# Kernel tuning notes

Measured on AMD Instinct MI355X. Metric: run time of the kernel, lower is better.

## Reference

```python
import jax, jax.numpy as jnp
import numpy as np

B, S, DM, H, FF = 2, 2048, 1024, 16, 4096
DH = DM // H
EPS = 1e-5


def setup_inputs() -> dict:
    key = jax.random.key(0)
    ks = jax.random.split(key, 16)
    s = 0.02
    return {
        "x": jax.random.normal(ks[0], (B, S, DM), jnp.float32),
        "mask": jnp.ones((B, S), jnp.int32),
        "Wq": jax.random.normal(ks[1], (DM, DM), jnp.float32) * s,
        "bq": jnp.zeros((DM,), jnp.float32),
        "Wk": jax.random.normal(ks[2], (DM, DM), jnp.float32) * s,
        "bk": jnp.zeros((DM,), jnp.float32),
        "Wv": jax.random.normal(ks[3], (DM, DM), jnp.float32) * s,
        "bv": jnp.zeros((DM,), jnp.float32),
        "Wo": jax.random.normal(ks[4], (DM, DM), jnp.float32) * s,
        "bo": jnp.zeros((DM,), jnp.float32),
        "W1": jax.random.normal(ks[5], (DM, FF), jnp.float32) * s,
        "b1": jnp.zeros((FF,), jnp.float32),
        "W2": jax.random.normal(ks[6], (FF, DM), jnp.float32) * s,
        "b2": jnp.zeros((DM,), jnp.float32),
        "g1": jnp.ones((DM,), jnp.float32),
        "beta1": jnp.zeros((DM,), jnp.float32),
        "g2": jnp.ones((DM,), jnp.float32),
        "beta2": jnp.zeros((DM,), jnp.float32),
    }


def _layer_norm(x, g, b):
    mu = jnp.mean(x, axis=-1, keepdims=True)
    var = jnp.var(x, axis=-1, keepdims=True)
    return (x - mu) * jax.lax.rsqrt(var + EPS) * g + b


def reference(x, mask, Wq, bq, Wk, bk, Wv, bv, Wo, bo, W1, b1, W2, b2, g1, beta1, g2, beta2):
    # --- hollow multi-head attention ---
    q = (x @ Wq + bq).reshape(B, S, H, DH)
    k = (x @ Wk + bk).reshape(B, S, H, DH)
    v = (x @ Wv + bv).reshape(B, S, H, DH)
    scores = jnp.einsum("bqhd,bkhd->bhqk", q, k) / jnp.sqrt(jnp.float32(DH))
    # triu(diag=1) and tril(diag=-1) masks kill everything off-diagonal
    diag = jnp.eye(S, dtype=bool)  # [S, S]
    scores = jnp.where(diag[None, None], scores, -jnp.inf)
    attn = jax.nn.softmax(scores, axis=-1)
    out = jnp.einsum("bhqk,bkhd->bqhd", attn, v).reshape(B, S, DM)
    attn_out = out @ Wo + bo
    # --- residual + LN1 ---
    h = _layer_norm(x + attn_out, g1, beta1)
    # --- FFN ---
    ff = jax.nn.relu(h @ W1 + b1) @ W2 + b2
    # --- residual + LN2 ---
    return _layer_norm(h + ff, g2, beta2)
```

## Files before the change

kernel.cpp:

```cpp
#include <hip/hip_runtime.h>
#include <stdint.h>

typedef __bf16 bf16x8 __attribute__((ext_vector_type(8)));
typedef float f32x4 __attribute__((ext_vector_type(4)));

__device__ __forceinline__ uint16_t f2bf(float f) {
  union { float f; uint32_t u; } c; c.f = f;
  uint32_t u = c.u;
  u += 0x7fffu + ((u >> 16) & 1u);
  return (uint16_t)(u >> 16);
}
__device__ __forceinline__ float bf2f(uint16_t u) {
  union { uint32_t u; float f; } c; c.u = (uint32_t)u << 16; return c.f;
}

__device__ __forceinline__ void cvt_body(const float* __restrict__ in,
                                         uint16_t* __restrict__ out, int i) {
  float4 v = reinterpret_cast<const float4*>(in)[i];
  ushort4 o;
  o.x = f2bf(v.x); o.y = f2bf(v.y); o.z = f2bf(v.z); o.w = f2bf(v.w);
  reinterpret_cast<ushort4*>(out)[i] = o;
}

__global__ void prep_kernel(const float* __restrict__ x, const float* __restrict__ Wv,
                            const float* __restrict__ Wo, const float* __restrict__ W1,
                            const float* __restrict__ W2, const float* __restrict__ bv,
                            const float* __restrict__ bo,
                            uint16_t* __restrict__ xb, uint16_t* __restrict__ wvb,
                            uint16_t* __restrict__ woT, uint16_t* __restrict__ w1t,
                            uint16_t* __restrict__ w2t, float* __restrict__ bc) {
  __shared__ float tsh[32][33];
  __shared__ float red[8][32];
  int b = blockIdx.x;
  const int t = threadIdx.x;
  if (b < 4096) { cvt_body(x, xb, b * 256 + t); return; }
  b -= 4096;
  if (b < 1024) { cvt_body(Wv, wvb, b * 256 + t); return; }
  b -= 1024;

  const float* tin = nullptr; uint16_t* tout = nullptr;
  int R = 0, C = 0, bx = 0, by = 0;
  if (b < 1024) {
    tin = Wo; tout = woT; R = 1024; C = 1024; bx = b & 31; by = b >> 5;
  } else if (b < 1024 + 4096) {
    const int bb = b - 1024;
    tin = W1; tout = w1t; R = 1024; C = 4096; bx = bb & 127; by = bb >> 7;
  } else if (b < 1024 + 8192) {
    const int bb = b - (1024 + 4096);
    tin = W2; tout = w2t; R = 4096; C = 1024; bx = bb & 31; by = bb >> 5;
  } else {
    const int jb = b - (1024 + 8192);
    const int jl = t & 31, kg = t >> 5;
    const int j = jb * 32 + jl;
    float s = 0.f;
    const int k0 = kg * 128;
    for (int k = k0; k < k0 + 128; ++k) s += bv[k] * Wo[(size_t)k * 1024 + j];
    red[kg][jl] = s;
    __syncthreads();
    if (kg == 0) {
      float acc = bo[j];
#pragma unroll
      for (int q = 0; q < 8; ++q) acc += red[q][jl];
      bc[j] = acc;
    }
    return;
  }
  const int tx = t & 31, ty = t >> 5;
  const int c0 = bx * 32, r0 = by * 32;
#pragma unroll
  for (int i = 0; i < 4; ++i)
    tsh[ty + i * 8][tx] = tin[(size_t)(r0 + ty + i * 8) * C + (c0 + tx)];
  __syncthreads();
#pragma unroll
  for (int i = 0; i < 4; ++i)
    tout[(size_t)(c0 + ty + i * 8) * R + (r0 + tx)] = f2bf(tsh[tx][ty + i * 8]);
}

constexpr int BM = 128, BN = 128, BK = 64;

template <int MODE>
__launch_bounds__(256, 2)
__global__ void gemm2ph_kernel(const uint16_t* __restrict__ A, const uint16_t* __restrict__ Bt,
                               const float* __restrict__ bias, const float* __restrict__ res,
                               void* __restrict__ out, int M, int N, int Klen, int lda, int ldb) {
  __shared__ uint16_t sAB[2][2][BM * BK];
  const int tid  = threadIdx.x;
  const int lane = tid & 63;
  const int wave = tid >> 6;

  const int nwg = gridDim.x * gridDim.y;
  int wg = blockIdx.y * gridDim.x + blockIdx.x;
  wg = (wg & 7) * (nwg >> 3) + (wg >> 3);
  const int bx = wg % gridDim.x, by = wg / gridDim.x;
  const int m0 = by * BM, n0 = bx * BN;

  const int wm = (wave >> 1) * 64;
  const int wn = (wave & 1) * 64;

  f32x4 acc[4][4] = {};

  const int srow = tid >> 3;
  const int scol = ((tid & 7) ^ (srow & 7)) * 8;
  const uint16_t* ga[4];
  const uint16_t* gb[4];
  uint32_t loff[4];
#pragma unroll
  for (int g = 0; g < 4; ++g) {
    const int row = srow + 32 * g;
    ga[g] = A + (size_t)(m0 + row) * lda + scol;
    gb[g] = Bt + (size_t)(n0 + row) * ldb + scol;
    loff[g] = (uint32_t)(tid + g * 256) * 8;
  }

  const int fr = lane & 15;
  const int hi = lane >> 4;
  const int rx = fr & 7;

  const int nk = Klen / BK;

#define STAGE2(buf, kt)                                                                   \
  {                                                                                       \
    _Pragma("unroll")                                                                     \
    for (int g = 0; g < 4; ++g) {                                                         \
      __builtin_amdgcn_global_load_lds(                                                   \
          (const __attribute__((address_space(1))) uint32_t*)(ga[g] + (size_t)(kt) * BK), \
          (__attribute__((address_space(3))) uint32_t*)(&sAB[buf][0][loff[g]]), 16, 0, 0);\
      __builtin_amdgcn_global_load_lds(                                                   \
          (const __attribute__((address_space(1))) uint32_t*)(gb[g] + (size_t)(kt) * BK), \
          (__attribute__((address_space(3))) uint32_t*)(&sAB[buf][1][loff[g]]), 16, 0, 0);\
    }                                                                                     \
  }

  STAGE2(0, 0);
  __syncthreads();

  int cur = 0;
  for (int kt = 0; kt < nk; ++kt) {
    if (kt + 1 < nk) STAGE2(cur ^ 1, kt + 1);
    const uint16_t* pA = &sAB[cur][0][0];
    const uint16_t* pB = &sAB[cur][1][0];
    bf16x8 af[4][2], bb[4][2];
#pragma unroll
    for (int m = 0; m < 4; ++m)
#pragma unroll
      for (int ks = 0; ks < 2; ++ks) {
        const int slot = (ks * 4 + hi) ^ rx;
        af[m][ks] = *reinterpret_cast<const bf16x8*>(pA + (wm + m * 16 + fr) * BK + slot * 8);
        bb[m][ks] = *reinterpret_cast<const bf16x8*>(pB + (wn + m * 16 + fr) * BK + slot * 8);
      }
#pragma unroll
    for (int ks = 0; ks < 2; ++ks)
#pragma unroll
      for (int m = 0; m < 4; ++m)
#pragma unroll
        for (int n = 0; n < 4; ++n)
          acc[m][n] = __builtin_amdgcn_mfma_f32_16x16x32_bf16(af[m][ks], bb[n][ks], acc[m][n], 0, 0, 0);
    __syncthreads();
    cur ^= 1;
  }
#undef STAGE2

  const int cn  = lane & 15;
  const int cm4 = (lane >> 4) * 4;
#pragma unroll
  for (int m = 0; m < 4; ++m) {
#pragma unroll
    for (int n = 0; n < 4; ++n) {
      const int gm = m0 + wm + m * 16 + cm4;
      const int gn = n0 + wn + n * 16 + cn;
      const float bbv = bias ? bias[gn] : 0.f;
#pragma unroll
      for (int r = 0; r < 4; ++r) {
        const size_t idx = (size_t)(gm + r) * N + gn;
        const float vv = acc[m][n][r] + bbv;
        if constexpr (MODE == 0) {
          ((uint16_t*)out)[idx] = f2bf(vv);
        } else {
          ((uint16_t*)out)[idx] = f2bf(vv + res[idx]);
        }
      }
    }
  }
}

template <int MODE>
__launch_bounds__(512, 2)
__global__ void gemm8ph_kernel(const uint16_t* __restrict__ A, const uint16_t* __restrict__ Bt,
                               const float* __restrict__ bias, void* __restrict__ out,
                               int M, int N, int Klen, int lda, int ldb) {
  extern __shared__ uint16_t lds[];
  const int tid  = threadIdx.x;
  const int lane = tid & 63;
  const int wave = tid >> 6;

  const int nwg = gridDim.x * gridDim.y;
  int wg = blockIdx.y * gridDim.x + blockIdx.x;
  wg = (wg & 7) * (nwg >> 3) + (wg >> 3);
  const int bx = wg % gridDim.x, by = wg / gridDim.x;
  const int m0 = by * 256, n0 = bx * 256;

  const int z = blockIdx.z;
  A  += (size_t)z * Klen;
  Bt += (size_t)z * Klen;

  const int wm = (wave >> 2) * 128;
  const int wn = (wave & 3) * 64;

  f32x4 acc[8][4] = {};

  const int srw = tid >> 3;
  const int sp  = tid & 7;
  const uint16_t* gu[8];
#pragma unroll
  for (int u = 0; u < 8; ++u) {
    const uint16_t* base = (u < 4) ? A + (size_t)(m0 + u * 64) * lda
                                   : Bt + (size_t)(n0 + (u - 4) * 64) * ldb;
    const int ld = (u < 4) ? lda : ldb;
    gu[u] = base + (size_t)srw * ld + ((sp ^ (srw & 7)) * 8);
  }

  const int nk = Klen / 64;

#define STAGE8(T, U)                                                                          \
  if ((T) < nk) {                                                                             \
    __builtin_amdgcn_global_load_lds(                                                         \
        (const __attribute__((address_space(1))) uint32_t*)(gu[U] + (size_t)(T) * 64),        \
        (__attribute__((address_space(3))) uint32_t*)(lds + ((T) & 1) * 32768 + (U) * 4096 +  \
                                                      tid * 8),                               \
        16, 0, 0);                                                                            \
  }

  const int fr = lane & 15;
  const int hi = lane >> 4;
  int aoff[8];
#pragma unroll
  for (int m = 0; m < 8; ++m) {
    const int u = (wm >> 6) + (m >> 2);
    const int R = (m & 3) * 16 + fr;
    aoff[m] = u * 4096 + R * 64 + ((hi ^ (R & 7)) * 8);
  }
  int boff[4];
#pragma unroll
  for (int n = 0; n < 4; ++n) {
    const int u = 4 + (wn >> 6);
    const int R = n * 16 + fr;
    boff[n] = u * 4096 + R * 64 + ((hi ^ (R & 7)) * 8);
  }

  STAGE8(0, 0); STAGE8(0, 1); STAGE8(0, 2); STAGE8(0, 3);
  STAGE8(0, 4); STAGE8(0, 5); STAGE8(0, 6); STAGE8(0, 7);
  STAGE8(1, 4); STAGE8(1, 5); STAGE8(1, 6); STAGE8(1, 7);
  asm volatile("s_waitcnt vmcnt(4)" ::: "memory");
  __builtin_amdgcn_s_barrier();

#define LD8(off) (*reinterpret_cast<const bf16x8*>(bufp + (off)))
#define PHASE_MFMA32(KS)                                                      \
  __builtin_amdgcn_s_setprio(1);                                              \
  _Pragma("unroll") for (int mm = 0; mm < 8; ++mm)                            \
    _Pragma("unroll") for (int n = 0; n < 4; ++n)                             \
      acc[mm][n] = __builtin_amdgcn_mfma_f32_16x16x32_bf16(                   \
          aq[mm], bq[n][KS], acc[mm][n], 0, 0, 0);                            \
  __builtin_amdgcn_s_setprio(0);

  for (int k = 0; k < nk; ++k) {
    const uint16_t* bufp = lds + (k & 1) * 32768;
    bf16x8 bq[4][2], aq[8];
#pragma unroll
    for (int n = 0; n < 4; ++n) { bq[n][0] = LD8(boff[n]); bq[n][1] = LD8(boff[n] ^ 32); }
#pragma unroll
    for (int mm = 0; mm < 8; ++mm) aq[mm] = LD8(aoff[mm]);
    STAGE8(k + 1, 0); STAGE8(k + 1, 1); STAGE8(k + 1, 2); STAGE8(k + 1, 3);
    PHASE_MFMA32(0);
    asm volatile("s_waitcnt lgkmcnt(0)" ::: "memory");
    __builtin_amdgcn_s_barrier();
#pragma unroll
    for (int mm = 0; mm < 8; ++mm) aq[mm] = LD8(aoff[mm] ^ 32);
    STAGE8(k + 2, 4); STAGE8(k + 2, 5); STAGE8(k + 2, 6); STAGE8(k + 2, 7);
    PHASE_MFMA32(1);
    if (k < nk - 2) { asm volatile("s_waitcnt vmcnt(4)" ::: "memory"); }
    else            { asm volatile("s_waitcnt vmcnt(0)" ::: "memory"); }
    asm volatile("s_waitcnt lgkmcnt(0)" ::: "memory");
    __builtin_amdgcn_s_barrier();
  }
#undef PHASE_MFMA32
#undef LD8
#undef STAGE8

  const int cn  = lane & 15;
  const int cm4 = (lane >> 4) * 4;
  uint16_t* outp = (uint16_t*)out;
  if constexpr (MODE == 1) outp += (size_t)z * M * N;
  float bias_n[4];
  if constexpr (MODE == 0) {
#pragma unroll
    for (int n = 0; n < 4; ++n) bias_n[n] = bias[n0 + wn + n * 16 + cn];
  }
#pragma unroll
  for (int m = 0; m < 8; ++m) {
#pragma unroll
    for (int n = 0; n < 4; ++n) {
      const int gm = m0 + wm + m * 16 + cm4;
      const int gn = n0 + wn + n * 16 + cn;
#pragma unroll
      for (int r = 0; r < 4; ++r) {
        const size_t idx = (size_t)(gm + r) * N + gn;
        if constexpr (MODE == 0) {
          outp[idx] = f2bf(fmaxf(acc[m][n][r] + bias_n[n], 0.f));
        } else {
          outp[idx] = f2bf(acc[m][n][r]);
        }
      }
    }
  }
}

__global__ void ln1_kernel(const uint16_t* __restrict__ in,
                           const float* __restrict__ g,
                           const float* __restrict__ b,
                           uint16_t* __restrict__ outb) {
  const int row = blockIdx.x;
  const int t = threadIdx.x;
  const ushort4 r4 = reinterpret_cast<const ushort4*>(in + (size_t)row * 1024)[t];
  float4 v;
  v.x = bf2f(r4.x); v.y = bf2f(r4.y); v.z = bf2f(r4.z); v.w = bf2f(r4.w);
  float s  = v.x + v.y + v.z + v.w;
  float s2 = v.x * v.x + v.y * v.y + v.z * v.z + v.w * v.w;
#pragma unroll
  for (int o = 32; o > 0; o >>= 1) { s += __shfl_down(s, o); s2 += __shfl_down(s2, o); }
  __shared__ float red[8];
  const int lane = t & 63, wave = t >> 6;
  if (lane == 0) { red[wave] = s; red[4 + wave] = s2; }
  __syncthreads();
  const float S  = red[0] + red[1] + red[2] + red[3];
  const float S2 = red[4] + red[5] + red[6] + red[7];
  const float mu  = S * (1.f / 1024.f);
  const float var = S2 * (1.f / 1024.f) - mu * mu;
  const float rs  = rsqrtf(var + 1e-5f);
  const float4 gg = reinterpret_cast<const float4*>(g)[t];
  const float4 bb = reinterpret_cast<const float4*>(b)[t];
  ushort4 ob;
  ob.x = f2bf((v.x - mu) * rs * gg.x + bb.x);
  ob.y = f2bf((v.y - mu) * rs * gg.y + bb.y);
  ob.z = f2bf((v.z - mu) * rs * gg.z + bb.z);
  ob.w = f2bf((v.w - mu) * rs * gg.w + bb.w);
  reinterpret_cast<ushort4*>(outb + (size_t)row * 1024)[t] = ob;
}

__global__ void ln2_kernel(const uint16_t* __restrict__ pp, size_t pstride,
                           const uint16_t* __restrict__ hb, const float* __restrict__ b2,
                           const float* __restrict__ g, const float* __restrict__ be,
                           float* __restrict__ out) {
  const int row = blockIdx.x;
  const int t = threadIdx.x;
  const size_t base = (size_t)row * 1024;
  const ushort4 h4 = reinterpret_cast<const ushort4*>(hb + base)[t];
  const float4 c2 = reinterpret_cast<const float4*>(b2)[t];
  float4 v;
  v.x = c2.x + bf2f(h4.x); v.y = c2.y + bf2f(h4.y);
  v.z = c2.z + bf2f(h4.z); v.w = c2.w + bf2f(h4.w);
#pragma unroll
  for (int zz = 0; zz < 4; ++zz) {
    const ushort4 p4 = reinterpret_cast<const ushort4*>(pp + zz * pstride + base)[t];
    v.x += bf2f(p4.x); v.y += bf2f(p4.y); v.z += bf2f(p4.z); v.w += bf2f(p4.w);
  }
  float s  = v.x + v.y + v.z + v.w;
  float s2 = v.x * v.x + v.y * v.y + v.z * v.z + v.w * v.w;
#pragma unroll
  for (int o = 32; o > 0; o >>= 1) { s += __shfl_down(s, o); s2 += __shfl_down(s2, o); }
  __shared__ float red[8];
  const int lane = t & 63, wave = t >> 6;
  if (lane == 0) { red[wave] = s; red[4 + wave] = s2; }
  __syncthreads();
  const float S  = red[0] + red[1] + red[2] + red[3];
  const float S2 = red[4] + red[5] + red[6] + red[7];
  const float mu  = S * (1.f / 1024.f);
  const float var = S2 * (1.f / 1024.f) - mu * mu;
  const float rs  = rsqrtf(var + 1e-5f);
  const float4 gg = reinterpret_cast<const float4*>(g)[t];
  const float4 bb = reinterpret_cast<const float4*>(be)[t];
  float4 o;
  o.x = (v.x - mu) * rs * gg.x + bb.x;
  o.y = (v.y - mu) * rs * gg.y + bb.y;
  o.z = (v.z - mu) * rs * gg.z + bb.z;
  o.w = (v.w - mu) * rs * gg.w + bb.w;
  reinterpret_cast<float4*>(out + base)[t] = o;
}

extern "C" void kernel_launch(void* const* d_in, const int* in_sizes, int n_in,
                              void* d_out, int out_size, void* d_ws, size_t ws_size,
                              hipStream_t stream) {
  const float* x   = (const float*)d_in[0];
  const float* Wv  = (const float*)d_in[6];
  const float* bv  = (const float*)d_in[7];
  const float* Wo  = (const float*)d_in[8];
  const float* bo  = (const float*)d_in[9];
  const float* W1  = (const float*)d_in[10];
  const float* b1  = (const float*)d_in[11];
  const float* W2  = (const float*)d_in[12];
  const float* b2  = (const float*)d_in[13];
  const float* g1  = (const float*)d_in[14];
  const float* be1 = (const float*)d_in[15];
  const float* g2  = (const float*)d_in[16];
  const float* be2 = (const float*)d_in[17];
  float* out = (float*)d_out;

  constexpr int M = 4096, DM = 1024, FF = 4096;

  char* p = (char*)d_ws;
  auto alloc = [&](size_t bytes) {
    char* r = p;
    p += (bytes + 255) & ~(size_t)255;
    return r;
  };
  uint16_t* xb  = (uint16_t*)alloc((size_t)M * DM * 2);
  uint16_t* wvb = (uint16_t*)alloc((size_t)DM * DM * 2);
  uint16_t* woT = (uint16_t*)alloc((size_t)DM * DM * 2);
  uint16_t* w1t = (uint16_t*)alloc((size_t)FF * DM * 2);
  uint16_t* w2t = (uint16_t*)alloc((size_t)DM * FF * 2);
  uint16_t* wcT = (uint16_t*)alloc((size_t)DM * DM * 2);
  float*    bc  = (float*)   alloc((size_t)DM * 4);
  uint16_t* r1b = (uint16_t*)alloc((size_t)M * DM * 2);
  uint16_t* hb  = (uint16_t*)alloc((size_t)M * DM * 2);
  uint16_t* tb  = (uint16_t*)alloc((size_t)M * FF * 2);
  uint16_t* pp  = (uint16_t*)alloc((size_t)4 * M * DM * 2);

  (void)hipFuncSetAttribute(reinterpret_cast<const void*>(gemm8ph_kernel<0>),
                            hipFuncAttributeMaxDynamicSharedMemorySize, 131072);
  (void)hipFuncSetAttribute(reinterpret_cast<const void*>(gemm8ph_kernel<1>),
                            hipFuncAttributeMaxDynamicSharedMemorySize, 131072);

  prep_kernel<<<4096 + 1024 + 1024 + 4096 + 4096 + 32, 256, 0, stream>>>(
      x, Wv, Wo, W1, W2, bv, bo, xb, wvb, woT, w1t, w2t, bc);

  gemm2ph_kernel<0><<<dim3(DM / BN, DM / BM), 256, 0, stream>>>(
      woT, wvb, nullptr, nullptr, wcT, DM, DM, DM, DM, DM);
  gemm2ph_kernel<1><<<dim3(DM / BN, M / BM), 256, 0, stream>>>(
      xb, wcT, bc, x, r1b, M, DM, DM, DM, DM);
  ln1_kernel<<<M, 256, 0, stream>>>(r1b, g1, be1, hb);
  gemm8ph_kernel<0><<<dim3(FF / 256, M / 256), 512, 131072, stream>>>(
      hb, w1t, b1, tb, M, FF, DM, DM, DM);
  gemm8ph_kernel<1><<<dim3(DM / 256, M / 256, 4), 512, 131072, stream>>>(
      tb, w2t, nullptr, pp, M, DM, FF / 4, FF, FF);
  ln2_kernel<<<M, 256, 0, stream>>>(pp, (size_t)M * DM, hb, b2, g2, be2, out);
}
```

Measured before the change: 143.2 us.

## Replace 256x256 FFN GEMM with smaller-tile, higher-occupancy 128x256 kernel

The FFN GEMMs move from a 256x256 tile with 128KB of dynamic LDS and a two-phase K=64 pipeline to a 128x256 tile with K=32 steps and static double-buffered LDS of 48KB. Launch bounds rise to 4 blocks per CU and the grid doubles in the M dimension. The aim is more resident waves to hide latency and better CU fill for these fairly small GEMMs. In exchange, per-tile reuse drops and the loop waits for all loads with vmcnt(0) on every iteration, so there is more global traffic and less overlap inside each block.

New measurement: 150.8 us. 5.4% more time.

```diff
diff --git a/kernel.cpp b/kernel.cpp
--- a/kernel.cpp
+++ b/kernel.cpp
@@ -184,11 +184,12 @@
 }
 
 template <int MODE>
-__launch_bounds__(512, 2)
-__global__ void gemm8ph_kernel(const uint16_t* __restrict__ A, const uint16_t* __restrict__ Bt,
+__launch_bounds__(512, 4)
+__global__ void gemm_hi_kernel(const uint16_t* __restrict__ A, const uint16_t* __restrict__ Bt,
                                const float* __restrict__ bias, void* __restrict__ out,
                                int M, int N, int Klen, int lda, int ldb) {
-  extern __shared__ uint16_t lds[];
+  __shared__ uint16_t sA[2][128 * 32];
+  __shared__ uint16_t sB[2][256 * 32];
   const int tid  = threadIdx.x;
   const int lane = tid & 63;
   const int wave = tid >> 6;
@@ -197,94 +198,77 @@
   int wg = blockIdx.y * gridDim.x + blockIdx.x;
   wg = (wg & 7) * (nwg >> 3) + (wg >> 3);
   const int bx = wg % gridDim.x, by = wg / gridDim.x;
-  const int m0 = by * 256, n0 = bx * 256;
+  const int m0 = by * 128, n0 = bx * 256;
 
   const int z = blockIdx.z;
   A  += (size_t)z * Klen;
   Bt += (size_t)z * Klen;
 
-  const int wm = (wave >> 2) * 128;
+  const int wm = (wave >> 2) * 64;
   const int wn = (wave & 3) * 64;
 
-  f32x4 acc[8][4] = {};
-
-  const int srw = tid >> 3;
-  const int sp  = tid & 7;
-  const uint16_t* gu[8];
-#pragma unroll
-  for (int u = 0; u < 8; ++u) {
-    const uint16_t* base = (u < 4) ? A + (size_t)(m0 + u * 64) * lda
-                                   : Bt + (size_t)(n0 + (u - 4) * 64) * ldb;
-    const int ld = (u < 4) ? lda : ldb;
-    gu[u] = base + (size_t)srw * ld + ((sp ^ (srw & 7)) * 8);
-  }
-
-  const int nk = Klen / 64;
-
-#define STAGE8(T, U)                                                                          \
-  if ((T) < nk) {                                                                             \
-    __builtin_amdgcn_global_load_lds(                                                         \
-        (const __attribute__((address_space(1))) uint32_t*)(gu[U] + (size_t)(T) * 64),        \
-        (__attribute__((address_space(3))) uint32_t*)(lds + ((T) & 1) * 32768 + (U) * 4096 +  \
-                                                      tid * 8),                               \
-        16, 0, 0);                                                                            \
+  f32x4 acc[4][4] = {};
+
+  const int srw = tid >> 2;
+  const int sp  = tid & 3;
+  const int skey = (srw >> 1) & 3;
+  const uint16_t* gA  = A  + (size_t)(m0 + srw) * lda + ((sp ^ skey) * 8);
+  const uint16_t* gB0 = Bt + (size_t)(n0 + srw) * ldb + ((sp ^ skey) * 8);
+  const uint16_t* gB1 = gB0 + (size_t)128 * ldb;
+
+  const int nk = Klen / 32;
+
+#define STG(T, buf)                                                                         \
+  {                                                                                         \
+    __builtin_amdgcn_global_load_lds(                                                       \
+        (const __attribute__((address_space(1))) uint32_t*)(gA + (size_t)(T) * 32),         \
+        (__attribute__((address_space(3))) uint32_t*)(&sA[buf][tid * 8]), 16, 0, 0);        \
+    __builtin_amdgcn_global_load_lds(                                                       \
+        (const __attribute__((address_space(1))) uint32_t*)(gB0 + (size_t)(T) * 32),        \
+        (__attribute__((address_space(3))) uint32_t*)(&sB[buf][tid * 8]), 16, 0, 0);        \
+    __builtin_amdgcn_global_load_lds(                                                       \
+        (const __attribute__((address_space(1))) uint32_t*)(gB1 + (size_t)(T) * 32),        \
+        (__attribute__((address_space(3))) uint32_t*)(&sB[buf][(tid + 512) * 8]), 16, 0, 0);\
   }
 
   const int fr = lane & 15;
   const int hi = lane >> 4;
-  int aoff[8];
-#pragma unroll
-  for (int m = 0; m < 8; ++m) {
-    const int u = (wm >> 6) + (m >> 2);
-    const int R = (m & 3) * 16 + fr;
-    aoff[m] = u * 4096 + R * 64 + ((hi ^ (R & 7)) * 8);
-  }
-  int boff[4];
+  int aoff[4], boff[4];
+#pragma unroll
+  for (int m = 0; m < 4; ++m) {
+    const int R = wm + m * 16 + fr;
+    aoff[m] = R * 32 + ((hi ^ ((R >> 1) & 3)) * 8);
+  }
 #pragma unroll
   for (int n = 0; n < 4; ++n) {
-    const int u = 4 + (wn >> 6);
-    const int R = n * 16 + fr;
-    boff[n] = u * 4096 + R * 64 + ((hi ^ (R & 7)) * 8);
-  }
-
-  STAGE8(0, 0); STAGE8(0, 1); STAGE8(0, 2); STAGE8(0, 3);
-  STAGE8(0, 4); STAGE8(0, 5); STAGE8(0, 6); STAGE8(0, 7);
-  STAGE8(1, 4); STAGE8(1, 5); STAGE8(1, 6); STAGE8(1, 7);
-  asm volatile("s_waitcnt vmcnt(4)" ::: "memory");
+    const int R = wn + n * 16 + fr;
+    boff[n] = R * 32 + ((hi ^ ((R >> 1) & 3)) * 8);
+  }
+
+  STG(0, 0);
+  asm volatile("s_waitcnt vmcnt(0)" ::: "memory");
   __builtin_amdgcn_s_barrier();
 
-#define LD8(off) (*reinterpret_cast<const bf16x8*>(bufp + (off)))
-#define PHASE_MFMA32(KS)                                                      \
-  __builtin_amdgcn_s_setprio(1);                                              \
-  _Pragma("unroll") for (int mm = 0; mm < 8; ++mm)                            \
-    _Pragma("unroll") for (int n = 0; n < 4; ++n)                             \
-      acc[mm][n] = __builtin_amdgcn_mfma_f32_16x16x32_bf16(                   \
-          aq[mm], bq[n][KS], acc[mm][n], 0, 0, 0);                            \
-  __builtin_amdgcn_s_setprio(0);
-
   for (int k = 0; k < nk; ++k) {
-    const uint16_t* bufp = lds + (k & 1) * 32768;
-    bf16x8 bq[4][2], aq[8];
-#pragma unroll
-    for (int n = 0; n < 4; ++n) { bq[n][0] = LD8(boff[n]); bq[n][1] = LD8(boff[n] ^ 32); }
-#pragma unroll
-    for (int mm = 0; mm < 8; ++mm) aq[mm] = LD8(aoff[mm]);
-    STAGE8(k + 1, 0); STAGE8(k + 1, 1); STAGE8(k + 1, 2); STAGE8(k + 1, 3);
-    PHASE_MFMA32(0);
+    const int cur = k & 1;
+    if (k + 1 < nk) STG(k + 1, cur ^ 1);
+    bf16x8 aq[4], bq[4];
+#pragma unroll
+    for (int m = 0; m < 4; ++m) aq[m] = *reinterpret_cast<const bf16x8*>(&sA[cur][aoff[m]]);
+#pragma unroll
+    for (int n = 0; n < 4; ++n) bq[n] = *reinterpret_cast<const bf16x8*>(&sB[cur][boff[n]]);
+    __builtin_amdgcn_s_setprio(1);
+#pragma unroll
+    for (int m = 0; m < 4; ++m)
+#pragma unroll
+      for (int n = 0; n < 4; ++n)
+        acc[m][n] = __builtin_amdgcn_mfma_f32_16x16x32_bf16(aq[m], bq[n], acc[m][n], 0, 0, 0);
+    __builtin_amdgcn_s_setprio(0);
+    asm volatile("s_waitcnt vmcnt(0)" ::: "memory");
     asm volatile("s_waitcnt lgkmcnt(0)" ::: "memory");
     __builtin_amdgcn_s_barrier();
-#pragma unroll
-    for (int mm = 0; mm < 8; ++mm) aq[mm] = LD8(aoff[mm] ^ 32);
-    STAGE8(k + 2, 4); STAGE8(k + 2, 5); STAGE8(k + 2, 6); STAGE8(k + 2, 7);
-    PHASE_MFMA32(1);
-    if (k < nk - 2) { asm volatile("s_waitcnt vmcnt(4)" ::: "memory"); }
-    else            { asm volatile("s_waitcnt vmcnt(0)" ::: "memory"); }
-    asm volatile("s_waitcnt lgkmcnt(0)" ::: "memory");
-    __builtin_amdgcn_s_barrier();
-  }
-#undef PHASE_MFMA32
-#undef LD8
-#undef STAGE8
+  }
+#undef STG
 
   const int cn  = lane & 15;
   const int cm4 = (lane >> 4) * 4;
@@ -296,7 +280,7 @@
     for (int n = 0; n < 4; ++n) bias_n[n] = bias[n0 + wn + n * 16 + cn];
   }
 #pragma unroll
-  for (int m = 0; m < 8; ++m) {
+  for (int m = 0; m < 4; ++m) {
 #pragma unroll
     for (int n = 0; n < 4; ++n) {
       const int gm = m0 + wm + m * 16 + cm4;
@@ -424,11 +408,6 @@
   uint16_t* tb  = (uint16_t*)alloc((size_t)M * FF * 2);
   uint16_t* pp  = (uint16_t*)alloc((size_t)4 * M * DM * 2);
 
-  (void)hipFuncSetAttribute(reinterpret_cast<const void*>(gemm8ph_kernel<0>),
-                            hipFuncAttributeMaxDynamicSharedMemorySize, 131072);
-  (void)hipFuncSetAttribute(reinterpret_cast<const void*>(gemm8ph_kernel<1>),
-                            hipFuncAttributeMaxDynamicSharedMemorySize, 131072);
-
   prep_kernel<<<4096 + 1024 + 1024 + 4096 + 4096 + 32, 256, 0, stream>>>(
       x, Wv, Wo, W1, W2, bv, bo, xb, wvb, woT, w1t, w2t, bc);
 
@@ -437,9 +416,9 @@
   gemm2ph_kernel<1><<<dim3(DM / BN, M / BM), 256, 0, stream>>>(
       xb, wcT, bc, x, r1b, M, DM, DM, DM, DM);
   ln1_kernel<<<M, 256, 0, stream>>>(r1b, g1, be1, hb);
-  gemm8ph_kernel<0><<<dim3(FF / 256, M / 256), 512, 131072, stream>>>(
+  gemm_hi_kernel<0><<<dim3(FF / 256, M / 128), 512, 0, stream>>>(
       hb, w1t, b1, tb, M, FF, DM, DM, DM);
-  gemm8ph_kernel<1><<<dim3(DM / 256, M / 256, 4), 512, 131072, stream>>>(
+  gemm_hi_kernel<1><<<dim3(DM / 256, M / 128, 4), 512, 0, stream>>>(
       tb, w2t, nullptr, pp, M, DM, FF / 4, FF, FF);
   ln2_kernel<<<M, 256, 0, stream>>>(pp, (size_t)M * DM, hb, b2, g2, be2, out);
 }
```

## Split-K the weight-combine and attention-output GEMMs and fuse residual into LN1

Applied to the files above, without the earlier changes.

The Wo·Wv weight product is now split four ways along K with a small reduction kernel. The x·Wc GEMM is split two ways along K, and its partials, bias and residual are summed inside LN1. This gives the small-grid GEMMs more workgroups to fill the GPU (the 1024×1024 product previously launched only 64 tiles). The cost is extra partial-sum traffic, one more kernel launch, and rounding each partial to bf16. The residual also changes from the fp32 x to the bf16 xb, which slightly alters precision.

Measured after the change: 138.8 us (median of 2 runs). -3.0%, faster.

```diff
diff --git a/kernel.cpp b/kernel.cpp
--- a/kernel.cpp
+++ b/kernel.cpp
@@ -94,6 +94,10 @@
   const int bx = wg % gridDim.x, by = wg / gridDim.x;
   const int m0 = by * BM, n0 = bx * BN;
 
+  const int z = blockIdx.z;
+  A  += (size_t)z * Klen;
+  Bt += (size_t)z * Klen;
+
   const int wm = (wave >> 1) * 64;
   const int wn = (wave & 1) * 64;
 
@@ -162,6 +166,7 @@
 
   const int cn  = lane & 15;
   const int cm4 = (lane >> 4) * 4;
+  uint16_t* outp = (uint16_t*)out + (size_t)z * M * N;
 #pragma unroll
   for (int m = 0; m < 4; ++m) {
 #pragma unroll
@@ -174,13 +179,28 @@
         const size_t idx = (size_t)(gm + r) * N + gn;
         const float vv = acc[m][n][r] + bbv;
         if constexpr (MODE == 0) {
-          ((uint16_t*)out)[idx] = f2bf(vv);
+          outp[idx] = f2bf(vv);
         } else {
           ((uint16_t*)out)[idx] = f2bf(vv + res[idx]);
         }
       }
     }
   }
+}
+
+__global__ void comb4_kernel(const uint16_t* __restrict__ wp, size_t stride,
+                             uint16_t* __restrict__ o, int n4) {
+  const int i = blockIdx.x * 256 + threadIdx.x;
+  if (i >= n4) return;
+  float4 v = {0.f, 0.f, 0.f, 0.f};
+#pragma unroll
+  for (int zz = 0; zz < 4; ++zz) {
+    const ushort4 p = reinterpret_cast<const ushort4*>(wp + zz * stride)[i];
+    v.x += bf2f(p.x); v.y += bf2f(p.y); v.z += bf2f(p.z); v.w += bf2f(p.w);
+  }
+  ushort4 r;
+  r.x = f2bf(v.x); r.y = f2bf(v.y); r.z = f2bf(v.z); r.w = f2bf(v.w);
+  reinterpret_cast<ushort4*>(o)[i] = r;
 }
 
 template <int MODE>
@@ -314,15 +334,22 @@
   }
 }
 
-__global__ void ln1_kernel(const uint16_t* __restrict__ in,
-                           const float* __restrict__ g,
-                           const float* __restrict__ b,
+__global__ void ln1_kernel(const uint16_t* __restrict__ q0, const uint16_t* __restrict__ q1,
+                           const uint16_t* __restrict__ xb, const float* __restrict__ bc,
+                           const float* __restrict__ g, const float* __restrict__ b,
                            uint16_t* __restrict__ outb) {
   const int row = blockIdx.x;
   const int t = threadIdx.x;
-  const ushort4 r4 = reinterpret_cast<const ushort4*>(in + (size_t)row * 1024)[t];
+  const size_t base = (size_t)row * 1024;
+  const ushort4 a4 = reinterpret_cast<const ushort4*>(q0 + base)[t];
+  const ushort4 b4 = reinterpret_cast<const ushort4*>(q1 + base)[t];
+  const ushort4 x4 = reinterpret_cast<const ushort4*>(xb + base)[t];
+  const float4 c4 = reinterpret_cast<const float4*>(bc)[t];
   float4 v;
-  v.x = bf2f(r4.x); v.y = bf2f(r4.y); v.z = bf2f(r4.z); v.w = bf2f(r4.w);
+  v.x = bf2f(a4.x) + bf2f(b4.x) + bf2f(x4.x) + c4.x;
+  v.y = bf2f(a4.y) + bf2f(b4.y) + bf2f(x4.y) + c4.y;
+  v.z = bf2f(a4.z) + bf2f(b4.z) + bf2f(x4.z) + c4.z;
+  v.w = bf2f(a4.w) + bf2f(b4.w) + bf2f(x4.w) + c4.w;
   float s  = v.x + v.y + v.z + v.w;
   float s2 = v.x * v.x + v.y * v.y + v.z * v.z + v.w * v.w;
 #pragma unroll
@@ -343,7 +370,7 @@
   ob.y = f2bf((v.y - mu) * rs * gg.y + bb.y);
   ob.z = f2bf((v.z - mu) * rs * gg.z + bb.z);
   ob.w = f2bf((v.w - mu) * rs * gg.w + bb.w);
-  reinterpret_cast<ushort4*>(outb + (size_t)row * 1024)[t] = ob;
+  reinterpret_cast<ushort4*>(outb + base)[t] = ob;
 }
 
 __global__ void ln2_kernel(const uint16_t* __restrict__ pp, size_t pstride,
@@ -419,10 +446,11 @@
   uint16_t* w2t = (uint16_t*)alloc((size_t)DM * FF * 2);
   uint16_t* wcT = (uint16_t*)alloc((size_t)DM * DM * 2);
   float*    bc  = (float*)   alloc((size_t)DM * 4);
-  uint16_t* r1b = (uint16_t*)alloc((size_t)M * DM * 2);
   uint16_t* hb  = (uint16_t*)alloc((size_t)M * DM * 2);
   uint16_t* tb  = (uint16_t*)alloc((size_t)M * FF * 2);
   uint16_t* pp  = (uint16_t*)alloc((size_t)4 * M * DM * 2);
+  uint16_t* wp = pp;
+  uint16_t* q  = tb;
 
   (void)hipFuncSetAttribute(reinterpret_cast<const void*>(gemm8ph_kernel<0>),
                             hipFuncAttributeMaxDynamicSharedMemorySize, 131072);
@@ -432,11 +460,12 @@
   prep_kernel<<<4096 + 1024 + 1024 + 4096 + 4096 + 32, 256, 0, stream>>>(
       x, Wv, Wo, W1, W2, bv, bo, xb, wvb, woT, w1t, w2t, bc);
 
-  gemm2ph_kernel<0><<<dim3(DM / BN, DM / BM), 256, 0, stream>>>(
-      woT, wvb, nullptr, nullptr, wcT, DM, DM, DM, DM, DM);
-  gemm2ph_kernel<1><<<dim3(DM / BN, M / BM), 256, 0, stream>>>(
-      xb, wcT, bc, x, r1b, M, DM, DM, DM, DM);
-  ln1_kernel<<<M, 256, 0, stream>>>(r1b, g1, be1, hb);
+  gemm2ph_kernel<0><<<dim3(DM / BN, DM / BM, 4), 256, 0, stream>>>(
+      woT, wvb, nullptr, nullptr, wp, DM, DM, DM / 4, DM, DM);
+  comb4_kernel<<<DM * DM / 4 / 256, 256, 0, stream>>>(wp, (size_t)DM * DM, wcT, DM * DM / 4);
+  gemm2ph_kernel<0><<<dim3(DM / BN, M / BM, 2), 256, 0, stream>>>(
+      xb, wcT, nullptr, nullptr, q, M, DM, DM / 2, DM, DM);
+  ln1_kernel<<<M, 256, 0, stream>>>(q, q + (size_t)M * DM, xb, bc, g1, be1, hb);
   gemm8ph_kernel<0><<<dim3(FF / 256, M / 256), 512, 131072, stream>>>(
       hb, w1t, b1, tb, M, FF, DM, DM, DM);
   gemm8ph_kernel<1><<<dim3(DM / 256, M / 256, 4), 512, 131072, stream>>>(
```
